# Kernel tuning notes

Hardware: AMD Instinct MI355X
Metric: run time of the kernel (lower is better)

## Reference

```python
import jax, jax.numpy as jnp
import numpy as np

B = 4           # batchsize == poolsize, pool = arange(B)
N_NODES = 32768
N_EDGES = 262144
CH_V = 16
CH_E = 16
HID = 64
CH_MSG = 2 * CH_V + CH_E  # 48


def setup_inputs() -> dict:
    key = jax.random.key(0)
    ks = jax.random.split(key, 8)
    node_vals = jax.random.normal(ks[0], (B, N_NODES, CH_V), jnp.float32) * 0.01
    edge_vals = jax.random.normal(ks[1], (B, N_EDGES, CH_E), jnp.float32) * 0.1
    conn_a = jax.random.randint(ks[2], (N_EDGES,), 0, N_NODES)
    conn_b = jax.random.randint(ks[3], (N_EDGES,), 0, N_NODES)
    w = lambda k, sh: jax.random.normal(k, sh, jnp.float32) * 0.1
    return {
        "node_vals": node_vals, "edge_vals": edge_vals,
        "conn_a": conn_a, "conn_b": conn_b,
        "Wm1": w(ks[4], (CH_MSG, HID)), "bm1": jnp.zeros((HID,), jnp.float32),
        "Wm2": w(ks[5], (HID, CH_MSG)), "bm2": jnp.zeros((CH_MSG,), jnp.float32),
        "Wu1": w(ks[6], (3 * CH_V, HID)), "bu1": jnp.zeros((HID,), jnp.float32),
        "Wu2": w(ks[7], (HID, CH_V)), "bu2": jnp.zeros((CH_V,), jnp.float32),
    }


def reference(node_vals, edge_vals, conn_a, conn_b,
              Wm1, bm1, Wm2, bm2, Wu1, bu1, Wu2, bu2):
    # NeuralGraph.timestep with node_dropout_p = edge_dropout_p = 0 (masks are identity),
    # use_update=True, average_messages=True, nodes=True, edges=True.
    h_a = node_vals[:, conn_a]                      # [B, E, CH_V] gather at source nodes
    h_b = node_vals[:, conn_b]                      # [B, E, CH_V] gather at target nodes
    h = jnp.concatenate([h_a, h_b, edge_vals], -1)  # [B, E, 48]
    # message MLP (Linear -> tanh -> Linear)
    m = jnp.tanh(h @ Wm1 + bm1) @ Wm2 + bm2         # [B, E, 48]
    m_a = m[..., :CH_V]
    m_b = m[..., CH_V:2 * CH_V]
    m_ab = m[..., 2 * CH_V:]
    # scatter-add aggregation per node (index_add_ along node dim)
    agg_a = jnp.zeros((B, N_NODES, CH_V), m.dtype).at[:, conn_a].add(m_a)
    agg_b = jnp.zeros((B, N_NODES, CH_V), m.dtype).at[:, conn_b].add(m_b)
    # count-based averaging (counts clamped to >= 1, matching the buffer fixup)
    ones = jnp.ones((N_EDGES,), m.dtype)
    cnt_a = jnp.maximum(jax.ops.segment_sum(ones, conn_a, num_segments=N_NODES), 1.0)
    cnt_b = jnp.maximum(jax.ops.segment_sum(ones, conn_b, num_segments=N_NODES), 1.0)
    agg_a = agg_a / cnt_a[None, :, None]
    agg_b = agg_b / cnt_b[None, :, None]
    # update MLP
    u_in = jnp.concatenate([agg_a, agg_b, node_vals], -1)   # [B, N, 48]
    updates = jnp.tanh(u_in @ Wu1 + bu1) @ Wu2 + bu2        # [B, N, CH_V]
    new_node_vals = node_vals + updates
    new_edge_vals = edge_vals + m_ab
    return new_node_vals, new_edge_vals
```

## Files before the change

kernel.cpp:

```cpp
#include <hip/hip_runtime.h>
#include <hip/hip_bf16.h>
#include <cstdint>
#include <cstddef>

#define B 4
#define NN 32768
#define NE 262144
#define CV 16
#define CE 16
#define HID 64
#define CM 48
#define HS 72

using frag  = __attribute__((ext_vector_type(8))) short;
using f32x4 = __attribute__((ext_vector_type(4))) float;

__device__ __forceinline__ float fast_tanh(float x) {
    float e = __expf(2.0f * x);
    return 1.0f - 2.0f / (e + 1.0f);
}

__device__ __forceinline__ unsigned short f2bf(float x) {
    union { float f; unsigned u; } v; v.f = x;
    unsigned r = (v.u + 0x7FFFu + ((v.u >> 16) & 1u)) >> 16;
    return (unsigned short)r;
}

__device__ __forceinline__ float bf2f(unsigned short x) {
    union { unsigned u; float f; } v; v.u = ((unsigned)x) << 16;
    return v.f;
}

__device__ __forceinline__ unsigned pk2bf(float lo, float hi) {
    union { __hip_bfloat162 h; unsigned u; } v;
    v.h = __float22bfloat162_rn(make_float2(lo, hi));
    return v.u;
}

__global__ __launch_bounds__(256) void count_kernel(
    const int* __restrict__ ca, const int* __restrict__ cb,
    int* __restrict__ cnt_a, int* __restrict__ cnt_b,
    int* __restrict__ rank_a, int* __restrict__ rank_b,
    const float* __restrict__ Wm1, const float* __restrict__ bm1,
    const float* __restrict__ Wm2,
    unsigned short* __restrict__ pW1, unsigned short* __restrict__ pW2)
{
    int i = blockIdx.x * 256 + threadIdx.x;
    rank_a[i] = atomicAdd(&cnt_a[ca[i]], 1);
    rank_b[i] = atomicAdd(&cnt_b[cb[i]], 1);

    if (blockIdx.x == 0) {
        for (int x = threadIdx.x; x < 4 * 2 * 64 * 8; x += 256) {
            int j = x & 7, lane = (x >> 3) & 63, ks = (x >> 9) & 1, mt = x >> 10;
            int m = mt * 16 + (lane & 15);
            int k = ks * 32 + (lane >> 4) * 8 + j;
            float w = (k < 48) ? Wm1[k * 64 + m] : (k == 48 ? bm1[m] : 0.0f);
            pW1[x] = f2bf(w);
        }
    } else if (blockIdx.x == 1) {
        for (int x = threadIdx.x; x < 3 * 2 * 64 * 8; x += 256) {
            int j = x & 7, lane = (x >> 3) & 63, ks = (x >> 9) & 1, mt = x >> 10;
            int m = mt * 16 + (lane & 15);
            int k = ks * 32 + (lane >> 4) * 8 + j;
            pW2[x] = f2bf(Wm2[k * 48 + m]);
        }
    }
}

__global__ __launch_bounds__(1024) void scan_kernel(
    const int* __restrict__ cnt_a, int* __restrict__ start_a,
    const int* __restrict__ cnt_b, int* __restrict__ start_b)
{
    const int* cnt = (blockIdx.x == 0) ? cnt_a : cnt_b;
    int* start     = (blockIdx.x == 0) ? start_a : start_b;

    __shared__ int s[1024];
    int t = threadIdx.x;
    int base = t * 32;
    int local[32];
    int sum = 0;
#pragma unroll
    for (int i = 0; i < 32; i++) { local[i] = cnt[base + i]; sum += local[i]; }
    s[t] = sum;
    __syncthreads();
    for (int off = 1; off < 1024; off <<= 1) {
        int add = (t >= off) ? s[t - off] : 0;
        __syncthreads();
        s[t] += add;
        __syncthreads();
    }
    int run = s[t] - sum;
#pragma unroll
    for (int i = 0; i < 32; i++) {
        start[base + i] = run;
        run += local[i];
    }
}

__global__ __launch_bounds__(256) void edge_kernel(
    const float* __restrict__ node_vals, const float* __restrict__ edge_vals,
    const int* __restrict__ ca, const int* __restrict__ cb,
    const int* __restrict__ rank_a, const int* __restrict__ rank_b,
    const int* __restrict__ start_a, const int* __restrict__ start_b,
    const unsigned short* __restrict__ pW1, const unsigned short* __restrict__ pW2,
    const float* __restrict__ bm2,
    float* __restrict__ out_edge,
    unsigned short* __restrict__ ma_csr, unsigned short* __restrict__ mb_csr)
{
    __shared__ unsigned short sH[256 * HS];
    __shared__ float sb2f[CM];

    int t = threadIdx.x;
    int lane = t & 63;
    int wv   = t >> 6;
    int col  = lane & 15;
    int quad = lane >> 4;
    int erow = wv * 64;
    int cha  = quad * 4;

    frag w1f[4][2];
#pragma unroll
    for (int mt = 0; mt < 4; mt++)
#pragma unroll
        for (int ks = 0; ks < 2; ks++)
            w1f[mt][ks] = *(const frag*)&pW1[(((mt * 2 + ks) * 64) + lane) * 8];

    if (t < CM) sb2f[t] = bm2[t];

    size_t eb = (size_t)blockIdx.x * 256;
    int posx, posy;
    {
        size_t idx = eb + t;
        int e = (int)(idx & (NE - 1));
        int bb = (int)(idx >> 18);
        int na = ca[e], nb = cb[e];
        posx = start_a[na] + rank_a[e];
        posy = start_b[nb] + rank_b[e];
        float h[48];
        const float4* pA = (const float4*)(node_vals + ((size_t)bb * NN + na) * CV);
        const float4* pB = (const float4*)(node_vals + ((size_t)bb * NN + nb) * CV);
        const float4* pE = (const float4*)(edge_vals + idx * CE);
#pragma unroll
        for (int q = 0; q < 4; q++) {
            float4 va = pA[q];
            h[q*4+0] = va.x; h[q*4+1] = va.y; h[q*4+2] = va.z; h[q*4+3] = va.w;
            float4 vb = pB[q];
            h[16+q*4+0] = vb.x; h[16+q*4+1] = vb.y; h[16+q*4+2] = vb.z; h[16+q*4+3] = vb.w;
            float4 ve = pE[q];
            h[32+q*4+0] = ve.x; h[32+q*4+1] = ve.y; h[32+q*4+2] = ve.z; h[32+q*4+3] = ve.w;
        }
        unsigned pk[32];
#pragma unroll
        for (int q = 0; q < 24; q++) pk[q] = pk2bf(h[2*q], h[2*q+1]);
        pk[24] = 0x3F80u;
#pragma unroll
        for (int q = 25; q < 32; q++) pk[q] = 0;
        uint4* row = (uint4*)&sH[t * HS];
        const uint4* src = (const uint4*)pk;
#pragma unroll
        for (int q = 0; q < 8; q++) row[q] = src[q];
    }
    __syncthreads();

    f32x4 acc1[4][4];
#pragma unroll
    for (int mt = 0; mt < 4; mt++)
#pragma unroll
        for (int nt = 0; nt < 4; nt++) acc1[mt][nt] = (f32x4){0.f, 0.f, 0.f, 0.f};

#pragma unroll
    for (int ks = 0; ks < 2; ks++) {
        frag bfr[4];
#pragma unroll
        for (int nt = 0; nt < 4; nt++)
            bfr[nt] = *(const frag*)&sH[(erow + nt*16 + col) * HS + ks*32 + quad*8];
#pragma unroll
        for (int mt = 0; mt < 4; mt++)
#pragma unroll
            for (int nt = 0; nt < 4; nt++)
                acc1[mt][nt] = __builtin_amdgcn_mfma_f32_16x16x32_bf16(w1f[mt][ks], bfr[nt], acc1[mt][nt], 0, 0, 0);
    }

    __syncthreads();

    frag w2f[3][2];
#pragma unroll
    for (int mt = 0; mt < 3; mt++)
#pragma unroll
        for (int ks = 0; ks < 2; ks++)
            w2f[mt][ks] = *(const frag*)&pW2[(((mt * 2 + ks) * 64) + lane) * 8];

#pragma unroll
    for (int nt = 0; nt < 4; nt++) {
        int row = erow + nt*16 + col;
#pragma unroll
        for (int mt = 0; mt < 4; mt++) {
            uint2 w;
            w.x = pk2bf(fast_tanh(acc1[mt][nt][0]), fast_tanh(acc1[mt][nt][1]));
            w.y = pk2bf(fast_tanh(acc1[mt][nt][2]), fast_tanh(acc1[mt][nt][3]));
            *(uint2*)&sH[row * HS + mt*16 + quad*4] = w;
        }
    }
    __syncthreads();

    f32x4 acc2[3][4];
#pragma unroll
    for (int mt = 0; mt < 3; mt++)
#pragma unroll
        for (int nt = 0; nt < 4; nt++) acc2[mt][nt] = (f32x4){0.f, 0.f, 0.f, 0.f};

#pragma unroll
    for (int ks = 0; ks < 2; ks++) {
        frag bfr[4];
#pragma unroll
        for (int nt = 0; nt < 4; nt++)
            bfr[nt] = *(const frag*)&sH[(erow + nt*16 + col) * HS + ks*32 + quad*8];
#pragma unroll
        for (int mt = 0; mt < 3; mt++)
#pragma unroll
            for (int nt = 0; nt < 4; nt++)
                acc2[mt][nt] = __builtin_amdgcn_mfma_f32_16x16x32_bf16(w2f[mt][ks], bfr[nt], acc2[mt][nt], 0, 0, 0);
    }

#pragma unroll
    for (int nt = 0; nt < 4; nt++) {
        int le = erow + nt*16 + col;
        size_t o = (eb + le) * CE + cha;
        float4 ev = *(const float4*)&edge_vals[o];
        float4 ov;
        ov.x = ev.x + acc2[2][nt][0] + sb2f[32+cha+0];
        ov.y = ev.y + acc2[2][nt][1] + sb2f[32+cha+1];
        ov.z = ev.z + acc2[2][nt][2] + sb2f[32+cha+2];
        ov.w = ev.w + acc2[2][nt][3] + sb2f[32+cha+3];
        *(float4*)&out_edge[o] = ov;
    }

    __syncthreads();

#pragma unroll
    for (int nt = 0; nt < 4; nt++) {
        int row = erow + nt*16 + col;
        uint2 wa;
        wa.x = pk2bf(acc2[0][nt][0] + sb2f[cha+0], acc2[0][nt][1] + sb2f[cha+1]);
        wa.y = pk2bf(acc2[0][nt][2] + sb2f[cha+2], acc2[0][nt][3] + sb2f[cha+3]);
        *(uint2*)&sH[row * HS + cha] = wa;
        uint2 wb;
        wb.x = pk2bf(acc2[1][nt][0] + sb2f[16+cha+0], acc2[1][nt][1] + sb2f[16+cha+1]);
        wb.y = pk2bf(acc2[1][nt][2] + sb2f[16+cha+2], acc2[1][nt][3] + sb2f[16+cha+3]);
        *(uint2*)&sH[row * HS + 16 + cha] = wb;
    }
    __syncthreads();

    {
        int bb = (int)((eb + t) >> 18);
        uint4 a0 = *(const uint4*)&sH[t * HS + 0];
        uint4 a1 = *(const uint4*)&sH[t * HS + 8];
        uint4 b0 = *(const uint4*)&sH[t * HS + 16];
        uint4 b1 = *(const uint4*)&sH[t * HS + 24];
        unsigned short* pa = &ma_csr[((size_t)bb * NE + posx) * 16];
        *(uint4*)(pa + 0) = a0;
        *(uint4*)(pa + 8) = a1;
        unsigned short* pb = &mb_csr[((size_t)bb * NE + posy) * 16];
        *(uint4*)(pb + 0) = b0;
        *(uint4*)(pb + 8) = b1;
    }
}

__global__ __launch_bounds__(256) void aggnode_kernel(
    const float* __restrict__ node_vals,
    const unsigned short* __restrict__ ma_csr, const unsigned short* __restrict__ mb_csr,
    const int* __restrict__ start_a, const int* __restrict__ start_b,
    const int* __restrict__ cnt_a, const int* __restrict__ cnt_b,
    const float* __restrict__ Wu1, const float* __restrict__ bu1,
    const float* __restrict__ Wu2, const float* __restrict__ bu2,
    float* __restrict__ out_node)
{
    __shared__ float sW1[HID * CM];
    __shared__ float sW2[HID * CV];
    __shared__ float sb1[HID];
    __shared__ float sb2[CV];
    __shared__ float aggL[256][33];

    int t = threadIdx.x;
    for (int x = t; x < HID * CM; x += 256) {
        int k = x / CM, i = x - k * CM;
        sW1[x] = Wu1[i * HID + k];
    }
    for (int x = t; x < HID * CV; x += 256) sW2[x] = Wu2[x];
    if (t < HID) sb1[t] = bu1[t];
    if (t < CV)  sb2[t] = bu2[t];

    int g0 = blockIdx.x * 256;
    int b  = g0 >> 15;

    int team = t >> 5;
    int half = (t >> 4) & 1;
    int l16  = t & 15;
    int e_off = l16 >> 2;
    int cg    = l16 & 3;

    const unsigned short* mcsr = half ? mb_csr : ma_csr;
    const int* stp  = half ? start_b : start_a;
    const int* cntp = half ? cnt_b   : cnt_a;

    for (int pass = 0; pass < 32; pass++) {
        int ln = pass * 8 + team;
        int n  = (g0 + ln) & (NN - 1);
        int d  = cntp[n];
        int s  = stp[n];
        const unsigned short* base = mcsr + ((size_t)b * NE + s) * 16 + cg * 4;
        float s0 = 0.f, s1 = 0.f, s2 = 0.f, s3 = 0.f;
        for (int k = e_off; k < d; k += 4) {
            uint2 v = *(const uint2*)(base + (size_t)k * 16);
            s0 += bf2f((unsigned short)(v.x & 0xFFFFu));
            s1 += bf2f((unsigned short)(v.x >> 16));
            s2 += bf2f((unsigned short)(v.y & 0xFFFFu));
            s3 += bf2f((unsigned short)(v.y >> 16));
        }
        s0 += __shfl_xor(s0, 4); s1 += __shfl_xor(s1, 4);
        s2 += __shfl_xor(s2, 4); s3 += __shfl_xor(s3, 4);
        s0 += __shfl_xor(s0, 8); s1 += __shfl_xor(s1, 8);
        s2 += __shfl_xor(s2, 8); s3 += __shfl_xor(s3, 8);
        if (e_off == 0) {
            float inv = 1.0f / (float)max(d, 1);
            float* dst = &aggL[ln][half * 16 + cg * 4];
            dst[0] = s0 * inv; dst[1] = s1 * inv; dst[2] = s2 * inv; dst[3] = s3 * inv;
        }
    }
    __syncthreads();

    int idx = g0 + t;
    float u[CM];
#pragma unroll
    for (int i = 0; i < 32; i++) u[i] = aggL[t][i];
    const float4* pn = (const float4*)(node_vals + (size_t)idx * CV);
#pragma unroll
    for (int q = 0; q < 4; q++) {
        float4 vn = pn[q];
        u[32+q*4+0] = vn.x; u[32+q*4+1] = vn.y; u[32+q*4+2] = vn.z; u[32+q*4+3] = vn.w;
    }

    float o[CV];
#pragma unroll
    for (int j = 0; j < CV; j++) o[j] = sb2[j];

    for (int k = 0; k < HID; k++) {
        float acc = sb1[k];
        const float* w1 = &sW1[k * CM];
#pragma unroll
        for (int i = 0; i < CM; i++) acc = fmaf(u[i], w1[i], acc);
        float th = fast_tanh(acc);
        const float* w2 = &sW2[k * CV];
#pragma unroll
        for (int j = 0; j < CV; j++) o[j] = fmaf(th, w2[j], o[j]);
    }

    float4* on = (float4*)(out_node + (size_t)idx * CV);
#pragma unroll
    for (int q = 0; q < 4; q++) {
        on[q] = make_float4(u[32+q*4+0] + o[q*4+0],
                            u[32+q*4+1] + o[q*4+1],
                            u[32+q*4+2] + o[q*4+2],
                            u[32+q*4+3] + o[q*4+3]);
    }
}

extern "C" void kernel_launch(void* const* d_in, const int* in_sizes, int n_in,
                              void* d_out, int out_size, void* d_ws, size_t ws_size,
                              hipStream_t stream) {
    const float* node_vals = (const float*)d_in[0];
    const float* edge_vals = (const float*)d_in[1];
    const int*   ca        = (const int*)d_in[2];
    const int*   cb        = (const int*)d_in[3];
    const float* Wm1 = (const float*)d_in[4];
    const float* bm1 = (const float*)d_in[5];
    const float* Wm2 = (const float*)d_in[6];
    const float* bm2 = (const float*)d_in[7];
    const float* Wu1 = (const float*)d_in[8];
    const float* bu1 = (const float*)d_in[9];
    const float* Wu2 = (const float*)d_in[10];
    const float* bu2 = (const float*)d_in[11];

    float* out_node = (float*)d_out;
    float* out_edge = out_node + (size_t)B * NN * CV;

    unsigned short* ma_csr = (unsigned short*)d_ws;
    unsigned short* mb_csr = ma_csr + (size_t)B * NE * 16;
    int* cnt_a   = (int*)(mb_csr + (size_t)B * NE * 16);
    int* cnt_b   = cnt_a + NN;
    int* start_a = cnt_b + NN;
    int* start_b = start_a + NN;
    int* rank_a  = start_b + NN;
    int* rank_b  = rank_a + NE;
    unsigned short* pW1 = (unsigned short*)(rank_b + NE);
    unsigned short* pW2 = pW1 + 4096;

    hipMemsetAsync(cnt_a, 0, 2 * (size_t)NN * sizeof(int), stream);

    count_kernel<<<NE / 256, 256, 0, stream>>>(
        ca, cb, cnt_a, cnt_b, rank_a, rank_b, Wm1, bm1, Wm2, pW1, pW2);
    scan_kernel<<<2, 1024, 0, stream>>>(cnt_a, start_a, cnt_b, start_b);
    edge_kernel<<<(B * NE) / 256, 256, 0, stream>>>(
        node_vals, edge_vals, ca, cb, rank_a, rank_b, start_a, start_b,
        pW1, pW2, bm2, out_edge, ma_csr, mb_csr);
    aggnode_kernel<<<(B * NN) / 256, 256, 0, stream>>>(
        node_vals, ma_csr, mb_csr, start_a, start_b, cnt_a, cnt_b,
        Wu1, bu1, Wu2, bu2, out_node);
}
```

Baseline: 337.6 us.

## Split CSR aggregation into its own kernel with one node per team

The fused aggregate-plus-update kernel is split into two kernels. The new agg_kernel gives each 32-thread team a single node and loads 16-byte rows with 8 edges in flight, then writes fp32 averages to global workspace. node_kernel reads those averages and runs the update MLP. This spreads the irregular gather over far more blocks and removes the 32-pass serial loop and its LDS staging, at the cost of an extra launch and a global round-trip for the aggregates (about 4 MB).

```diff
diff --git a/kernel.cpp b/kernel.cpp
--- a/kernel.cpp
+++ b/kernel.cpp
@@ -266,11 +266,63 @@
     }
 }
 
-__global__ __launch_bounds__(256) void aggnode_kernel(
-    const float* __restrict__ node_vals,
+__global__ __launch_bounds__(256) void agg_kernel(
     const unsigned short* __restrict__ ma_csr, const unsigned short* __restrict__ mb_csr,
     const int* __restrict__ start_a, const int* __restrict__ start_b,
     const int* __restrict__ cnt_a, const int* __restrict__ cnt_b,
+    float* __restrict__ agg_a, float* __restrict__ agg_b)
+{
+    int t = threadIdx.x;
+    int team = t >> 5;
+    int half = (t >> 4) & 1;
+    int l16  = t & 15;
+    int eoff  = l16 >> 1;
+    int chunk = l16 & 1;
+    int g = blockIdx.x * 8 + team;
+    int n = g & (NN - 1);
+    int b = g >> 15;
+
+    const unsigned short* mcsr = half ? mb_csr : ma_csr;
+    const int* stp  = half ? start_b : start_a;
+    const int* cntp = half ? cnt_b   : cnt_a;
+    float* aggp     = half ? agg_b   : agg_a;
+
+    int d = cntp[n];
+    int s = stp[n];
+    const unsigned short* base = mcsr + ((size_t)b * NE + s) * 16 + chunk * 8;
+
+    float acc[8] = {0.f, 0.f, 0.f, 0.f, 0.f, 0.f, 0.f, 0.f};
+    for (int k = eoff; k < d; k += 8) {
+        uint4 v = *(const uint4*)(base + (size_t)k * 16);
+        acc[0] += bf2f((unsigned short)(v.x & 0xFFFFu));
+        acc[1] += bf2f((unsigned short)(v.x >> 16));
+        acc[2] += bf2f((unsigned short)(v.y & 0xFFFFu));
+        acc[3] += bf2f((unsigned short)(v.y >> 16));
+        acc[4] += bf2f((unsigned short)(v.z & 0xFFFFu));
+        acc[5] += bf2f((unsigned short)(v.z >> 16));
+        acc[6] += bf2f((unsigned short)(v.w & 0xFFFFu));
+        acc[7] += bf2f((unsigned short)(v.w >> 16));
+    }
+#pragma unroll
+    for (int m = 2; m <= 8; m <<= 1) {
+#pragma unroll
+        for (int i = 0; i < 8; i++) acc[i] += __shfl_xor(acc[i], m);
+    }
+
+    if (eoff == 0) {
+        float inv = 1.0f / (float)max(d, 1);
+        float4 r0, r1;
+        r0.x = acc[0]*inv; r0.y = acc[1]*inv; r0.z = acc[2]*inv; r0.w = acc[3]*inv;
+        r1.x = acc[4]*inv; r1.y = acc[5]*inv; r1.z = acc[6]*inv; r1.w = acc[7]*inv;
+        float* dst = &aggp[(size_t)g * CV + chunk * 8];
+        *(float4*)(dst + 0) = r0;
+        *(float4*)(dst + 4) = r1;
+    }
+}
+
+__global__ __launch_bounds__(256) void node_kernel(
+    const float* __restrict__ node_vals,
+    const float* __restrict__ agg_a, const float* __restrict__ agg_b,
     const float* __restrict__ Wu1, const float* __restrict__ bu1,
     const float* __restrict__ Wu2, const float* __restrict__ bu2,
     float* __restrict__ out_node)
@@ -279,7 +331,6 @@
     __shared__ float sW2[HID * CV];
     __shared__ float sb1[HID];
     __shared__ float sb2[CV];
-    __shared__ float aggL[256][33];
 
     int t = threadIdx.x;
     for (int x = t; x < HID * CM; x += 256) {
@@ -289,53 +340,20 @@
     for (int x = t; x < HID * CV; x += 256) sW2[x] = Wu2[x];
     if (t < HID) sb1[t] = bu1[t];
     if (t < CV)  sb2[t] = bu2[t];
-
-    int g0 = blockIdx.x * 256;
-    int b  = g0 >> 15;
-
-    int team = t >> 5;
-    int half = (t >> 4) & 1;
-    int l16  = t & 15;
-    int e_off = l16 >> 2;
-    int cg    = l16 & 3;
-
-    const unsigned short* mcsr = half ? mb_csr : ma_csr;
-    const int* stp  = half ? start_b : start_a;
-    const int* cntp = half ? cnt_b   : cnt_a;
-
-    for (int pass = 0; pass < 32; pass++) {
-        int ln = pass * 8 + team;
-        int n  = (g0 + ln) & (NN - 1);
-        int d  = cntp[n];
-        int s  = stp[n];
-        const unsigned short* base = mcsr + ((size_t)b * NE + s) * 16 + cg * 4;
-        float s0 = 0.f, s1 = 0.f, s2 = 0.f, s3 = 0.f;
-        for (int k = e_off; k < d; k += 4) {
-            uint2 v = *(const uint2*)(base + (size_t)k * 16);
-            s0 += bf2f((unsigned short)(v.x & 0xFFFFu));
-            s1 += bf2f((unsigned short)(v.x >> 16));
-            s2 += bf2f((unsigned short)(v.y & 0xFFFFu));
-            s3 += bf2f((unsigned short)(v.y >> 16));
-        }
-        s0 += __shfl_xor(s0, 4); s1 += __shfl_xor(s1, 4);
-        s2 += __shfl_xor(s2, 4); s3 += __shfl_xor(s3, 4);
-        s0 += __shfl_xor(s0, 8); s1 += __shfl_xor(s1, 8);
-        s2 += __shfl_xor(s2, 8); s3 += __shfl_xor(s3, 8);
-        if (e_off == 0) {
-            float inv = 1.0f / (float)max(d, 1);
-            float* dst = &aggL[ln][half * 16 + cg * 4];
-            dst[0] = s0 * inv; dst[1] = s1 * inv; dst[2] = s2 * inv; dst[3] = s3 * inv;
-        }
-    }
-    __syncthreads();
-
-    int idx = g0 + t;
+    __syncthreads();
+
+    int idx = blockIdx.x * 256 + t;
+
     float u[CM];
-#pragma unroll
-    for (int i = 0; i < 32; i++) u[i] = aggL[t][i];
+    const float4* pa = (const float4*)(agg_a + (size_t)idx * CV);
+    const float4* pb = (const float4*)(agg_b + (size_t)idx * CV);
     const float4* pn = (const float4*)(node_vals + (size_t)idx * CV);
 #pragma unroll
     for (int q = 0; q < 4; q++) {
+        float4 va = pa[q];
+        u[q*4+0] = va.x; u[q*4+1] = va.y; u[q*4+2] = va.z; u[q*4+3] = va.w;
+        float4 vb = pb[q];
+        u[16+q*4+0] = vb.x; u[16+q*4+1] = vb.y; u[16+q*4+2] = vb.z; u[16+q*4+3] = vb.w;
         float4 vn = pn[q];
         u[32+q*4+0] = vn.x; u[32+q*4+1] = vn.y; u[32+q*4+2] = vn.z; u[32+q*4+3] = vn.w;
     }
@@ -386,7 +404,9 @@
 
     unsigned short* ma_csr = (unsigned short*)d_ws;
     unsigned short* mb_csr = ma_csr + (size_t)B * NE * 16;
-    int* cnt_a   = (int*)(mb_csr + (size_t)B * NE * 16);
+    float* agg_a = (float*)(mb_csr + (size_t)B * NE * 16);
+    float* agg_b = agg_a + (size_t)B * NN * CV;
+    int* cnt_a   = (int*)(agg_b + (size_t)B * NN * CV);
     int* cnt_b   = cnt_a + NN;
     int* start_a = cnt_b + NN;
     int* start_b = start_a + NN;
@@ -403,7 +423,8 @@
     edge_kernel<<<(B * NE) / 256, 256, 0, stream>>>(
         node_vals, edge_vals, ca, cb, rank_a, rank_b, start_a, start_b,
         pW1, pW2, bm2, out_edge, ma_csr, mb_csr);
-    aggnode_kernel<<<(B * NN) / 256, 256, 0, stream>>>(
-        node_vals, ma_csr, mb_csr, start_a, start_b, cnt_a, cnt_b,
-        Wu1, bu1, Wu2, bu2, out_node);
-}
+    agg_kernel<<<(B * NN) / 8, 256, 0, stream>>>(
+        ma_csr, mb_csr, start_a, start_b, cnt_a, cnt_b, agg_a, agg_b);
+    node_kernel<<<(B * NN) / 256, 256, 0, stream>>>(
+        node_vals, agg_a, agg_b, Wu1, bu1, Wu2, bu2, out_node);
+}
```

Result: faster. 323.2 us (-4.3%).
